# Kernel tuning notes

Hardware: AMD Instinct MI355X
Metric: run time of the kernel (lower is better)

## Reference

```python
import jax, jax.numpy as jnp
import numpy as np

L, B, S, D, H = 4, 4, 2048, 512, 8
DH = D // H
FF = 4 * D
BN_EPS = 1e-3  # keras BatchNormalization default epsilon


def setup_inputs() -> dict:
    key = jax.random.key(0)
    ks = jax.random.split(key, 8)
    g = lambda k, shape: jax.random.normal(k, shape, dtype=jnp.float32) * 0.02
    return {
        "sequence": jax.random.normal(ks[0], (B, S, D), dtype=jnp.float32),
        "wq": g(ks[1], (L, D, D)), "bq": jnp.zeros((L, D), jnp.float32),
        "wk": g(ks[2], (L, D, D)), "bk": jnp.zeros((L, D), jnp.float32),
        "wv": g(ks[3], (L, D, D)), "bv": jnp.zeros((L, D), jnp.float32),
        "wo": g(ks[4], (L, D, D)), "bo": jnp.zeros((L, D), jnp.float32),
        "w1": g(ks[5], (L, D, FF)), "b1": jnp.zeros((L, FF), jnp.float32),
        "w2": g(ks[6], (L, FF, D)), "b2": jnp.zeros((L, D), jnp.float32),
        "g1": jnp.ones((L, D), jnp.float32), "be1": jnp.zeros((L, D), jnp.float32),
        "g2": jnp.ones((L, D), jnp.float32), "be2": jnp.zeros((L, D), jnp.float32),
    }


def reference(sequence, wq, bq, wk, bk, wv, bv, wo, bo, w1, b1, w2, b2, g1, be1, g2, be2):
    # Inference-mode BatchNorm with moving_mean=0, moving_var=1:
    # bn(x) = x / sqrt(1 + eps) * gamma + beta
    bn_inv = 1.0 / jnp.sqrt(jnp.float32(1.0 + BN_EPS))
    scale = 1.0 / jnp.sqrt(jnp.float32(DH))
    x = sequence  # [B, S, D]
    for i in range(L):
        # Batched multi-head self-attention (== the per-position loop concat)
        q = (x @ wq[i] + bq[i]).reshape(B, S, H, DH)
        k = (x @ wk[i] + bk[i]).reshape(B, S, H, DH)
        v = (x @ wv[i] + bv[i]).reshape(B, S, H, DH)
        att = jax.nn.softmax(jnp.einsum('bqhd,bkhd->bhqk', q, k) * scale, axis=-1)
        o = jnp.einsum('bhqk,bkhd->bqhd', att, v).reshape(B, S, D)
        o = o @ wo[i] + bo[i]
        x = (x + o) * bn_inv * g1[i] + be1[i]          # residual + BN
        f = jax.nn.relu(x @ w1[i] + b1[i]) @ w2[i] + b2[i]  # FFN
        x = (x + f) * bn_inv * g2[i] + be2[i]          # residual + BN
    return x
```

## Files before the change

### kernel.cpp

```cpp
#include <hip/hip_runtime.h>
#include <hip/hip_bf16.h>

#define BB   4
#define SS   2048
#define DDIM 512
#define HH   8
#define DHD  64
#define FFD  2048
#define LLN  4
#define NQKV 1536
#define BN_INV 0.9995003747f
#define QSCALE 0.18033688011112042f

typedef __bf16 bf16x8 __attribute__((ext_vector_type(8)));
typedef __bf16 bf16x4 __attribute__((ext_vector_type(4)));
typedef float  f32x4  __attribute__((ext_vector_type(4)));

__device__ __forceinline__ void gl2lds16(const void* g, void* l) {
  __builtin_amdgcn_global_load_lds((const __attribute__((address_space(1))) void*)g,
                                   (__attribute__((address_space(3))) void*)l, 16, 0, 0);
}

__global__ __launch_bounds__(256) void k_transpose_w(const float* __restrict__ in,
                                                     __bf16* __restrict__ out,
                                                     int R, int C,
                                                     size_t in_zs, size_t out_zs) {
  __shared__ float tile[32][33];
  in += (size_t)blockIdx.z * in_zs;
  out += (size_t)blockIdx.z * out_zs;
  const int c0 = blockIdx.x * 32, r0 = blockIdx.y * 32;
  const int tx = threadIdx.x & 31, ty = threadIdx.x >> 5;
#pragma unroll
  for (int k = 0; k < 4; ++k) {
    int r = ty + k * 8;
    tile[r][tx] = in[(size_t)(r0 + r) * C + (c0 + tx)];
  }
  __syncthreads();
#pragma unroll
  for (int k = 0; k < 4; ++k) {
    int c = ty + k * 8;
    out[(size_t)(c0 + c) * R + (r0 + tx)] = (__bf16)tile[tx][c];
  }
}

__global__ __launch_bounds__(256) void k_bias_fuse(const float* __restrict__ bq,
                                                   const float* __restrict__ bk,
                                                   const float* __restrict__ bv,
                                                   float* __restrict__ out) {
  const int i = blockIdx.x * 256 + threadIdx.x;
  const int l = i / NQKV, j = i - l * NQKV;
  float v = (j < 512) ? bq[l * 512 + j]
          : (j < 1024) ? bk[l * 512 + j - 512]
                       : bv[l * 512 + j - 1024];
  out[i] = v;
}

__global__ __launch_bounds__(256) void k_transpose_v(const __bf16* __restrict__ qkv,
                                                     __bf16* __restrict__ vt) {
  __shared__ __bf16 tile[32][33];
  const int s0 = blockIdx.x * 32;
  const int d0 = blockIdx.y * 32;
  const int bh = blockIdx.z, b = bh >> 3, h = bh & 7;
  const int tx = threadIdx.x & 31, ty = threadIdx.x >> 5;
#pragma unroll
  for (int k = 0; k < 4; ++k) {
    int s = ty + k * 8;
    tile[s][tx] = qkv[(size_t)(b * SS + s0 + s) * NQKV + 2 * DDIM + h * DHD + d0 + tx];
  }
  __syncthreads();
#pragma unroll
  for (int k = 0; k < 4; ++k) {
    int d = ty + k * 8;
    vt[(size_t)(bh * DHD + d0 + d) * SS + (s0 + tx)] = tile[tx][d];
  }
}

__global__ __launch_bounds__(256) void k_cast(const float* __restrict__ in,
                                              float* __restrict__ xf,
                                              __bf16* __restrict__ xb) {
  const int i = (blockIdx.x * 256 + threadIdx.x) * 4;
  const float4 v = *(const float4*)(in + i);
  *(float4*)(xf + i) = v;
  bf16x4 o;
  o[0] = (__bf16)v.x; o[1] = (__bf16)v.y; o[2] = (__bf16)v.z; o[3] = (__bf16)v.w;
  *(bf16x4*)(xb + i) = o;
}

template <int EPI>
__global__ __launch_bounds__(256) void k_gemm_bt(const __bf16* __restrict__ A,
                                                 const __bf16* __restrict__ Bt,
                                                 const float* __restrict__ bias,
                                                 __bf16* __restrict__ Cb,
                                                 int M, int N, int K,
                                                 const float* __restrict__ xres,
                                                 float* __restrict__ xout,
                                                 const float* __restrict__ gvec,
                                                 const float* __restrict__ bvec) {
  __shared__ char As[128 * 128];
  __shared__ char Bs[128 * 128];
  const int tid = threadIdx.x;
  const int l = tid & 63, w = tid >> 6;
  const int wm = w >> 1, wn = w & 1;
  const int m0 = blockIdx.y * 128, n0 = blockIdx.x * 128;
  const int lr = l & 15, lg = l >> 4;
  f32x4 acc[4][4] = {};
  const int nk = K >> 6;
  const size_t ldab = (size_t)K * 2;
  for (int kt = 0; kt < nk; ++kt) {
    __syncthreads();
    const int k0b = kt * 128;
#pragma unroll
    for (int i = 0; i < 4; ++i) {
      const int chunk = i * 256 + tid;
      const int row = chunk >> 3;
      const int scb = ((chunk & 7) * 16) ^ ((row & 7) << 4);
      gl2lds16((const char*)A + (size_t)(m0 + row) * ldab + k0b + scb,
               As + (i * 256 + w * 64) * 16);
      gl2lds16((const char*)Bt + (size_t)(n0 + row) * ldab + k0b + scb,
               Bs + (i * 256 + w * 64) * 16);
    }
    __syncthreads();
#pragma unroll
    for (int kk = 0; kk < 2; ++kk) {
      bf16x8 a[4], b[4];
#pragma unroll
      for (int m = 0; m < 4; ++m) {
        const int row = wm * 64 + m * 16 + lr;
        const int cb = kk * 64 + lg * 16;
        a[m] = *(const bf16x8*)(As + row * 128 + (cb ^ ((row & 7) << 4)));
      }
#pragma unroll
      for (int n = 0; n < 4; ++n) {
        const int row = wn * 64 + n * 16 + lr;
        const int cb = kk * 64 + lg * 16;
        b[n] = *(const bf16x8*)(Bs + row * 128 + (cb ^ ((row & 7) << 4)));
      }
#pragma unroll
      for (int m = 0; m < 4; ++m)
#pragma unroll
        for (int n = 0; n < 4; ++n)
          acc[m][n] = __builtin_amdgcn_mfma_f32_16x16x32_bf16(a[m], b[n], acc[m][n], 0, 0, 0);
    }
  }
#pragma unroll
  for (int m = 0; m < 4; ++m) {
    const int gm = m0 + wm * 64 + m * 16 + lg * 4;
#pragma unroll
    for (int n = 0; n < 4; ++n) {
      const int gn = n0 + wn * 64 + n * 16 + lr;
      const float bv_ = bias[gn];
#pragma unroll
      for (int j = 0; j < 4; ++j) {
        const size_t idx = (size_t)(gm + j) * N + gn;
        float v = acc[m][n][j] + bv_;
        if constexpr (EPI == 1) {
          Cb[idx] = (__bf16)fmaxf(v, 0.0f);
        } else if constexpr (EPI == 2) {
          float t = (xres[idx] + v) * BN_INV * gvec[gn] + bvec[gn];
          xout[idx] = t;
          Cb[idx] = (__bf16)t;
        } else {
          if (gn < DDIM) v *= QSCALE;
          Cb[idx] = (__bf16)v;
        }
      }
    }
  }
}

__global__ __launch_bounds__(256, 2) void k_attn(const __bf16* __restrict__ QKV,
                                                 const __bf16* __restrict__ Vt,
                                                 __bf16* __restrict__ O) {
  __shared__ char smem[65536];
  char* Ks = smem;
  char* Vs = smem + 16384;
  char* Ps = smem + 32768;
  const int tid = threadIdx.x, l = tid & 63, w = tid >> 6;
  const int lr = l & 15, lg = l >> 4;
  const int bh = blockIdx.y, b = bh >> 3, h = bh & 7;
  const int q0 = blockIdx.x * 128 + w * 32;
  bf16x8 aq[2][2];
#pragma unroll
  for (int m = 0; m < 2; ++m) {
    const __bf16* qp = QKV + (size_t)(b * SS + q0 + m * 16 + lr) * NQKV + h * DHD + lg * 8;
    aq[m][0] = *(const bf16x8*)qp;
    aq[m][1] = *(const bf16x8*)(qp + 32);
  }
  f32x4 oacc[2][4] = {};
  float rsum[2][4] = {{0.f, 0.f, 0.f, 0.f}, {0.f, 0.f, 0.f, 0.f}};
  char* pw = Ps + w * 32 * 256;
  for (int t = 0; t < SS / 128; ++t) {
    __syncthreads();
    const int kv0 = t * 128;
#pragma unroll
    for (int i = 0; i < 4; ++i) {
      const int chunk = i * 256 + tid;
      const int row = chunk >> 3;
      const int scb = ((chunk & 7) * 16) ^ ((row & 7) << 4);
      gl2lds16((const char*)QKV + ((size_t)(b * SS + kv0 + row) * NQKV + DDIM + h * DHD) * 2 + scb,
               Ks + (i * 256 + w * 64) * 16);
    }
#pragma unroll
    for (int i = 0; i < 4; ++i) {
      const int chunk = i * 256 + tid;
      const int row = chunk >> 4;
      const int scb = ((chunk & 15) * 16) ^ ((row & 7) << 4);
      gl2lds16((const char*)Vt + ((size_t)(bh * DHD + row) * SS + kv0) * 2 + scb,
               Vs + (i * 256 + w * 64) * 16);
    }
    __syncthreads();
    f32x4 s[2][8];
#pragma unroll
    for (int n = 0; n < 8; ++n) {
      const int row = n * 16 + lr;
      const int swz = (row & 7) << 4;
      bf16x8 kf0 = *(const bf16x8*)(Ks + row * 128 + ((lg * 16) ^ swz));
      bf16x8 kf1 = *(const bf16x8*)(Ks + row * 128 + ((64 + lg * 16) ^ swz));
#pragma unroll
      for (int m = 0; m < 2; ++m) {
        f32x4 z = {};
        z = __builtin_amdgcn_mfma_f32_16x16x32_bf16(aq[m][0], kf0, z, 0, 0, 0);
        z = __builtin_amdgcn_mfma_f32_16x16x32_bf16(aq[m][1], kf1, z, 0, 0, 0);
        s[m][n] = z;
      }
    }
#pragma unroll
    for (int m = 0; m < 2; ++m)
#pragma unroll
      for (int n = 0; n < 8; ++n)
#pragma unroll
        for (int j = 0; j < 4; ++j) {
          const float p = __builtin_amdgcn_exp2f(s[m][n][j]);
          rsum[m][j] += p;
          const int r = m * 16 + lg * 4 + j;
          const int cb = (n * 16 + lr) * 2;
          *(__bf16*)(pw + r * 256 + (cb ^ ((r & 7) << 4))) = (__bf16)p;
        }
#pragma unroll
    for (int kk = 0; kk < 4; ++kk) {
      bf16x8 ap[2];
#pragma unroll
      for (int m = 0; m < 2; ++m) {
        const int r = m * 16 + lr;
        ap[m] = *(const bf16x8*)(pw + r * 256 + ((kk * 64 + lg * 16) ^ ((r & 7) << 4)));
      }
#pragma unroll
      for (int n = 0; n < 4; ++n) {
        const int row = n * 16 + lr;
        bf16x8 vf = *(const bf16x8*)(Vs + row * 256 + ((kk * 64 + lg * 16) ^ ((row & 7) << 4)));
#pragma unroll
        for (int m = 0; m < 2; ++m)
          oacc[m][n] = __builtin_amdgcn_mfma_f32_16x16x32_bf16(ap[m], vf, oacc[m][n], 0, 0, 0);
      }
    }
  }
#pragma unroll
  for (int m = 0; m < 2; ++m)
#pragma unroll
    for (int j = 0; j < 4; ++j) {
      float v = rsum[m][j];
      v += __shfl_xor(v, 1);
      v += __shfl_xor(v, 2);
      v += __shfl_xor(v, 4);
      v += __shfl_xor(v, 8);
      const float inv = 1.0f / v;
      const int sr = q0 + m * 16 + lg * 4 + j;
#pragma unroll
      for (int n = 0; n < 4; ++n)
        O[(size_t)(b * SS + sr) * DDIM + h * DHD + n * 16 + lr] = (__bf16)(oacc[m][n][j] * inv);
    }
}

static constexpr size_t SZ_WQKVT = (size_t)LLN * NQKV * DDIM * 2;
static constexpr size_t SZ_WOT   = (size_t)LLN * DDIM * DDIM * 2;
static constexpr size_t SZ_WT_DF = (size_t)LLN * DDIM * FFD * 2;
static constexpr size_t SZ_BQKV  = (size_t)LLN * NQKV * 4;
static constexpr size_t SZ_X     = (size_t)BB * SS * DDIM * 4;
static constexpr size_t SZ_ABF   = (size_t)BB * SS * DDIM * 2;
static constexpr size_t SZ_QKV   = (size_t)BB * SS * NQKV * 2;
static constexpr size_t OFF_WQKVT = 0;
static constexpr size_t OFF_WOT  = OFF_WQKVT + SZ_WQKVT;
static constexpr size_t OFF_W1T  = OFF_WOT + SZ_WOT;
static constexpr size_t OFF_W2T  = OFF_W1T + SZ_WT_DF;
static constexpr size_t OFF_BQKV = OFF_W2T + SZ_WT_DF;
static constexpr size_t OFF_X    = OFF_BQKV + SZ_BQKV;
static constexpr size_t OFF_XB   = OFF_X + SZ_X;
static constexpr size_t OFF_QKV  = OFF_XB + SZ_ABF;
static constexpr size_t OFF_VT   = OFF_QKV + SZ_QKV;
static constexpr size_t OFF_OB   = OFF_VT + SZ_ABF;
static constexpr size_t OFF_H1   = OFF_QKV;

extern "C" void kernel_launch(void* const* d_in, const int* in_sizes, int n_in,
                              void* d_out, int out_size, void* d_ws, size_t ws_size,
                              hipStream_t stream) {
  const float* seq = (const float*)d_in[0];
  const float* wq = (const float*)d_in[1];  const float* bq = (const float*)d_in[2];
  const float* wk = (const float*)d_in[3];  const float* bk = (const float*)d_in[4];
  const float* wv = (const float*)d_in[5];  const float* bv = (const float*)d_in[6];
  const float* wo = (const float*)d_in[7];  const float* bo = (const float*)d_in[8];
  const float* w1 = (const float*)d_in[9];  const float* b1 = (const float*)d_in[10];
  const float* w2 = (const float*)d_in[11]; const float* b2 = (const float*)d_in[12];
  const float* g1 = (const float*)d_in[13]; const float* be1 = (const float*)d_in[14];
  const float* g2 = (const float*)d_in[15]; const float* be2 = (const float*)d_in[16];

  char* ws = (char*)d_ws;
  __bf16* wqkvt = (__bf16*)(ws + OFF_WQKVT);
  __bf16* wot = (__bf16*)(ws + OFF_WOT);
  __bf16* w1t = (__bf16*)(ws + OFF_W1T);
  __bf16* w2t = (__bf16*)(ws + OFF_W2T);
  float*  bqkv = (float*)(ws + OFF_BQKV);
  float*  xf  = (float*)(ws + OFF_X);
  __bf16* xb  = (__bf16*)(ws + OFF_XB);
  __bf16* qkvb = (__bf16*)(ws + OFF_QKV);
  __bf16* vtb = (__bf16*)(ws + OFF_VT);
  __bf16* ob  = (__bf16*)(ws + OFF_OB);
  __bf16* h1  = (__bf16*)(ws + OFF_H1);

  const size_t zDD = (size_t)DDIM * DDIM;
  const size_t zQKV = (size_t)NQKV * DDIM;
  const size_t zDF = (size_t)DDIM * FFD;
  k_transpose_w<<<dim3(16, 16, LLN), 256, 0, stream>>>(wq, wqkvt, DDIM, DDIM, zDD, zQKV);
  k_transpose_w<<<dim3(16, 16, LLN), 256, 0, stream>>>(wk, wqkvt + (size_t)DDIM * DDIM, DDIM, DDIM, zDD, zQKV);
  k_transpose_w<<<dim3(16, 16, LLN), 256, 0, stream>>>(wv, wqkvt + (size_t)2 * DDIM * DDIM, DDIM, DDIM, zDD, zQKV);
  k_transpose_w<<<dim3(16, 16, LLN), 256, 0, stream>>>(wo, wot, DDIM, DDIM, zDD, zDD);
  k_transpose_w<<<dim3(64, 16, LLN), 256, 0, stream>>>(w1, w1t, DDIM, FFD, zDF, zDF);
  k_transpose_w<<<dim3(16, 64, LLN), 256, 0, stream>>>(w2, w2t, FFD, DDIM, zDF, zDF);
  k_bias_fuse<<<LLN * NQKV / 256, 256, 0, stream>>>(bq, bk, bv, bqkv);
  k_cast<<<4096, 256, 0, stream>>>(seq, xf, xb);

  const int M = BB * SS;
  for (int i = 0; i < LLN; ++i) {
    k_gemm_bt<3><<<dim3(NQKV / 128, M / 128), 256, 0, stream>>>(
        xb, wqkvt + (size_t)i * NQKV * DDIM, bqkv + i * NQKV, qkvb, M, NQKV, DDIM,
        nullptr, nullptr, nullptr, nullptr);
    k_transpose_v<<<dim3(SS / 32, DHD / 32, BB * HH), 256, 0, stream>>>(qkvb, vtb);
    k_attn<<<dim3(SS / 128, BB * HH), 256, 0, stream>>>(qkvb, vtb, ob);
    k_gemm_bt<2><<<dim3(DDIM / 128, M / 128), 256, 0, stream>>>(
        ob, wot + (size_t)i * DDIM * DDIM, bo + i * DDIM, xb, M, DDIM, DDIM,
        xf, xf, g1 + i * DDIM, be1 + i * DDIM);
    k_gemm_bt<1><<<dim3(FFD / 128, M / 128), 256, 0, stream>>>(
        xb, w1t + (size_t)i * DDIM * FFD, b1 + i * FFD, h1, M, FFD, DDIM,
        nullptr, nullptr, nullptr, nullptr);
    k_gemm_bt<2><<<dim3(DDIM / 128, M / 128), 256, 0, stream>>>(
        h1, w2t + (size_t)i * DDIM * FFD, b2 + i * DDIM, xb, M, DDIM, FFD,
        xf, (i == LLN - 1) ? (float*)d_out : xf, g2 + i * DDIM, be2 + i * DDIM);
  }
  (void)in_sizes; (void)n_in; (void)out_size; (void)ws_size;
}
```

Measured before the change: 710.9 us.

## Double-buffer LDS tiles in GEMM and attention, remap attention block order

```diff
diff --git a/kernel.cpp b/kernel.cpp
--- a/kernel.cpp
+++ b/kernel.cpp
@@ -96,8 +96,8 @@
                                                  float* __restrict__ xout,
                                                  const float* __restrict__ gvec,
                                                  const float* __restrict__ bvec) {
-  __shared__ char As[128 * 128];
-  __shared__ char Bs[128 * 128];
+  __shared__ char As[2][16384];
+  __shared__ char Bs[2][16384];
   const int tid = threadIdx.x;
   const int l = tid & 63, w = tid >> 6;
   const int wm = w >> 1, wn = w & 1;
@@ -106,8 +106,8 @@
   f32x4 acc[4][4] = {};
   const int nk = K >> 6;
   const size_t ldab = (size_t)K * 2;
-  for (int kt = 0; kt < nk; ++kt) {
-    __syncthreads();
+
+  auto stage = [&](int buf, int kt) {
     const int k0b = kt * 128;
 #pragma unroll
     for (int i = 0; i < 4; ++i) {
@@ -115,11 +115,17 @@
       const int row = chunk >> 3;
       const int scb = ((chunk & 7) * 16) ^ ((row & 7) << 4);
       gl2lds16((const char*)A + (size_t)(m0 + row) * ldab + k0b + scb,
-               As + (i * 256 + w * 64) * 16);
+               As[buf] + (i * 256 + w * 64) * 16);
       gl2lds16((const char*)Bt + (size_t)(n0 + row) * ldab + k0b + scb,
-               Bs + (i * 256 + w * 64) * 16);
-    }
-    __syncthreads();
+               Bs[buf] + (i * 256 + w * 64) * 16);
+    }
+  };
+
+  stage(0, 0);
+  __syncthreads();
+  int cur = 0;
+  for (int kt = 0; kt < nk; ++kt) {
+    if (kt + 1 < nk) stage(cur ^ 1, kt + 1);
 #pragma unroll
     for (int kk = 0; kk < 2; ++kk) {
       bf16x8 a[4], b[4];
@@ -127,13 +133,13 @@
       for (int m = 0; m < 4; ++m) {
         const int row = wm * 64 + m * 16 + lr;
         const int cb = kk * 64 + lg * 16;
-        a[m] = *(const bf16x8*)(As + row * 128 + (cb ^ ((row & 7) << 4)));
+        a[m] = *(const bf16x8*)(As[cur] + row * 128 + (cb ^ ((row & 7) << 4)));
       }
 #pragma unroll
       for (int n = 0; n < 4; ++n) {
         const int row = wn * 64 + n * 16 + lr;
         const int cb = kk * 64 + lg * 16;
-        b[n] = *(const bf16x8*)(Bs + row * 128 + (cb ^ ((row & 7) << 4)));
+        b[n] = *(const bf16x8*)(Bs[cur] + row * 128 + (cb ^ ((row & 7) << 4)));
       }
 #pragma unroll
       for (int m = 0; m < 4; ++m)
@@ -141,6 +147,9 @@
         for (int n = 0; n < 4; ++n)
           acc[m][n] = __builtin_amdgcn_mfma_f32_16x16x32_bf16(a[m], b[n], acc[m][n], 0, 0, 0);
     }
+    asm volatile("s_waitcnt vmcnt(0)" ::: "memory");
+    __syncthreads();
+    cur ^= 1;
   }
 #pragma unroll
   for (int m = 0; m < 4; ++m) {
@@ -171,14 +180,14 @@
 __global__ __launch_bounds__(256, 2) void k_attn(const __bf16* __restrict__ QKV,
                                                  const __bf16* __restrict__ Vt,
                                                  __bf16* __restrict__ O) {
-  __shared__ char smem[65536];
-  char* Ks = smem;
-  char* Vs = smem + 16384;
-  char* Ps = smem + 32768;
+  __shared__ char smem[81920];
   const int tid = threadIdx.x, l = tid & 63, w = tid >> 6;
   const int lr = l & 15, lg = l >> 4;
-  const int bh = blockIdx.y, b = bh >> 3, h = bh & 7;
-  const int q0 = blockIdx.x * 128 + w * 32;
+  const int f = blockIdx.y * 16 + blockIdx.x;
+  const int L = (f & 7) * 64 + (f >> 3);
+  const int qt = L & 15, bh = L >> 4;
+  const int b = bh >> 3, h = bh & 7;
+  const int q0 = qt * 128 + w * 32;
   bf16x8 aq[2][2];
 #pragma unroll
   for (int m = 0; m < 2; ++m) {
@@ -188,17 +197,19 @@
   }
   f32x4 oacc[2][4] = {};
   float rsum[2][4] = {{0.f, 0.f, 0.f, 0.f}, {0.f, 0.f, 0.f, 0.f}};
-  char* pw = Ps + w * 32 * 256;
-  for (int t = 0; t < SS / 128; ++t) {
-    __syncthreads();
+  char* pw = smem + 65536 + w * 4096;
+
+  auto stage = [&](int buf, int t) {
     const int kv0 = t * 128;
+    char* Kd = smem + buf * 16384;
+    char* Vd = smem + 32768 + buf * 16384;
 #pragma unroll
     for (int i = 0; i < 4; ++i) {
       const int chunk = i * 256 + tid;
       const int row = chunk >> 3;
       const int scb = ((chunk & 7) * 16) ^ ((row & 7) << 4);
       gl2lds16((const char*)QKV + ((size_t)(b * SS + kv0 + row) * NQKV + DDIM + h * DHD) * 2 + scb,
-               Ks + (i * 256 + w * 64) * 16);
+               Kd + (i * 256 + w * 64) * 16);
     }
 #pragma unroll
     for (int i = 0; i < 4; ++i) {
@@ -206,9 +217,17 @@
       const int row = chunk >> 4;
       const int scb = ((chunk & 15) * 16) ^ ((row & 7) << 4);
       gl2lds16((const char*)Vt + ((size_t)(bh * DHD + row) * SS + kv0) * 2 + scb,
-               Vs + (i * 256 + w * 64) * 16);
-    }
-    __syncthreads();
+               Vd + (i * 256 + w * 64) * 16);
+    }
+  };
+
+  stage(0, 0);
+  __syncthreads();
+  int cur = 0;
+  for (int t = 0; t < SS / 128; ++t) {
+    if (t < SS / 128 - 1) stage(cur ^ 1, t + 1);
+    const char* Ks = smem + cur * 16384;
+    const char* Vs = smem + 32768 + cur * 16384;
     f32x4 s[2][8];
 #pragma unroll
     for (int n = 0; n < 8; ++n) {
@@ -225,34 +244,41 @@
       }
     }
 #pragma unroll
-    for (int m = 0; m < 2; ++m)
-#pragma unroll
-      for (int n = 0; n < 8; ++n)
-#pragma unroll
-        for (int j = 0; j < 4; ++j) {
-          const float p = __builtin_amdgcn_exp2f(s[m][n][j]);
-          rsum[m][j] += p;
-          const int r = m * 16 + lg * 4 + j;
-          const int cb = (n * 16 + lr) * 2;
-          *(__bf16*)(pw + r * 256 + (cb ^ ((r & 7) << 4))) = (__bf16)p;
+    for (int hv = 0; hv < 2; ++hv) {
+#pragma unroll
+      for (int m = 0; m < 2; ++m)
+#pragma unroll
+        for (int nn = 0; nn < 4; ++nn)
+#pragma unroll
+          for (int j = 0; j < 4; ++j) {
+            const float p = __builtin_amdgcn_exp2f(s[m][hv * 4 + nn][j]);
+            rsum[m][j] += p;
+            const int r = m * 16 + lg * 4 + j;
+            const int cb = (nn * 16 + lr) * 2;
+            *(__bf16*)(pw + r * 128 + (cb ^ ((r & 7) << 4))) = (__bf16)p;
+          }
+#pragma unroll
+      for (int kk2 = 0; kk2 < 2; ++kk2) {
+        const int kkg = hv * 2 + kk2;
+        bf16x8 ap[2];
+#pragma unroll
+        for (int m = 0; m < 2; ++m) {
+          const int r = m * 16 + lr;
+          ap[m] = *(const bf16x8*)(pw + r * 128 + ((kk2 * 64 + lg * 16) ^ ((r & 7) << 4)));
         }
 #pragma unroll
-    for (int kk = 0; kk < 4; ++kk) {
-      bf16x8 ap[2];
-#pragma unroll
-      for (int m = 0; m < 2; ++m) {
-        const int r = m * 16 + lr;
-        ap[m] = *(const bf16x8*)(pw + r * 256 + ((kk * 64 + lg * 16) ^ ((r & 7) << 4)));
-      }
-#pragma unroll
-      for (int n = 0; n < 4; ++n) {
-        const int row = n * 16 + lr;
-        bf16x8 vf = *(const bf16x8*)(Vs + row * 256 + ((kk * 64 + lg * 16) ^ ((row & 7) << 4)));
-#pragma unroll
-        for (int m = 0; m < 2; ++m)
-          oacc[m][n] = __builtin_amdgcn_mfma_f32_16x16x32_bf16(ap[m], vf, oacc[m][n], 0, 0, 0);
-      }
-    }
+        for (int n = 0; n < 4; ++n) {
+          const int row = n * 16 + lr;
+          bf16x8 vf = *(const bf16x8*)(Vs + row * 256 + ((kkg * 64 + lg * 16) ^ ((row & 7) << 4)));
+#pragma unroll
+          for (int m = 0; m < 2; ++m)
+            oacc[m][n] = __builtin_amdgcn_mfma_f32_16x16x32_bf16(ap[m], vf, oacc[m][n], 0, 0, 0);
+        }
+      }
+    }
+    asm volatile("s_waitcnt vmcnt(0)" ::: "memory");
+    __syncthreads();
+    cur ^= 1;
   }
 #pragma unroll
   for (int m = 0; m < 2; ++m)
```

Result: faster. 680.2 us (-4.3%).
